# Kernel optimization log

Measured on AMD Instinct MI355X. Metric: run time of the kernel, lower is better.

## Reference

```python
import jax, jax.numpy as jnp
import numpy as np

L, D, H, DR, KF = 2, 256, 8, 64, 4   # n_layer, d_model, n_head, d_rpe, k_feedforward
B, S, T = 2, 256, 256
LN_EPS = 1e-5


def _ln(x, g, b):
    m = jnp.mean(x, -1, keepdims=True)
    v = jnp.mean((x - m) ** 2, -1, keepdims=True)
    return (x - m) * jax.lax.rsqrt(v + LN_EPS) * g + b


def _attn_rpe(q_in, kv_in, rpe, tgt_mask, wq, bq, wk, bk, wv, bv, wo, bo, wr, br):
    # RPE-biased multi-head cross attention: rpe -> (rpe_k, rpe_v) added per (src,tgt) pair.
    Bq, Sq, _ = q_in.shape
    Tk = kv_in.shape[1]
    Dh = D // H
    q = (q_in @ wq + bq).reshape(Bq, Sq, H, Dh)
    k = (kv_in @ wk + bk).reshape(Bq, Tk, H, Dh)
    v = (kv_in @ wv + bv).reshape(Bq, Tk, H, Dh)
    r = rpe @ wr + br                                   # [B,S,T,2D]
    rk, rv = jnp.split(r, 2, axis=-1)
    rk = rk.reshape(Bq, Sq, Tk, H, Dh)
    rv = rv.reshape(Bq, Sq, Tk, H, Dh)
    scale = 1.0 / np.sqrt(Dh).astype(np.float32)
    scores = (jnp.einsum('bshd,bthd->bhst', q, k)
              + jnp.einsum('bshd,bsthd->bhst', q, rk)) * scale
    scores = jnp.where(tgt_mask[:, None, None, :], -jnp.inf, scores)
    w = jax.nn.softmax(scores, axis=-1)                 # [B,H,S,T]
    out = (jnp.einsum('bhst,bthd->bshd', w, v)
           + jnp.einsum('bhst,bsthd->bshd', w, rv))
    return out.reshape(Bq, Sq, D) @ wo + bo


def _forward(src, tgt, rpe, src_padding_mask, tgt_padding_mask, p):
    for i in range(L):  # loop over n_layer (structurally distinct params)
        s2 = _ln(src, p['ln1_g'][i], p['ln1_b'][i])
        tn = _ln(tgt, p['lnt_g'][i], p['lnt_b'][i])
        a = _attn_rpe(s2, tn, rpe, tgt_padding_mask,
                      p['wq'][i], p['bq'][i], p['wk'][i], p['bk'][i],
                      p['wv'][i], p['bv'][i], p['wo'][i], p['bo'][i],
                      p['wr'][i], p['br'][i])
        src = src + a
        s2 = _ln(src, p['ln2_g'][i], p['ln2_b'][i])
        s2 = jax.nn.relu(s2 @ p['w1'][i] + p['b1'][i]) @ p['w2'][i] + p['b2'][i]
        src = src + s2
        src = jnp.where(src_padding_mask[:, :, None], 0.0, src)
    return src


def setup_inputs() -> dict:
    key = jax.random.key(0)
    ks = jax.random.split(key, 16)
    f = lambda k, shp: (0.02 * jax.random.normal(k, shp)).astype(jnp.float32)
    return {
        'src': jax.random.normal(ks[0], (B, S, D), jnp.float32),
        'tgt': jax.random.normal(ks[1], (B, T, D), jnp.float32),
        'rpe': jax.random.normal(ks[2], (B, S, T, DR), jnp.float32),
        'src_padding_mask': jax.random.bernoulli(ks[3], 0.05, (B, S)),
        'tgt_padding_mask': jax.random.bernoulli(ks[4], 0.1, (B, T)),
        'ln1_g': jnp.ones((L, D), jnp.float32), 'ln1_b': jnp.zeros((L, D), jnp.float32),
        'lnt_g': jnp.ones((L, D), jnp.float32), 'lnt_b': jnp.zeros((L, D), jnp.float32),
        'ln2_g': jnp.ones((L, D), jnp.float32), 'ln2_b': jnp.zeros((L, D), jnp.float32),
        'wq': f(ks[5], (L, D, D)), 'bq': jnp.zeros((L, D), jnp.float32),
        'wk': f(ks[6], (L, D, D)), 'bk': jnp.zeros((L, D), jnp.float32),
        'wv': f(ks[7], (L, D, D)), 'bv': jnp.zeros((L, D), jnp.float32),
        'wo': f(ks[8], (L, D, D)), 'bo': jnp.zeros((L, D), jnp.float32),
        'wr': f(ks[9], (L, DR, 2 * D)), 'br': jnp.zeros((L, 2 * D), jnp.float32),
        'w1': f(ks[10], (L, D, KF * D)), 'b1': jnp.zeros((L, KF * D), jnp.float32),
        'w2': f(ks[11], (L, KF * D, D)), 'b2': jnp.zeros((L, D), jnp.float32),
    }


def reference(src, tgt, rpe, src_padding_mask, tgt_padding_mask,
              ln1_g, ln1_b, lnt_g, lnt_b, ln2_g, ln2_b,
              wq, bq, wk, bk, wv, bv, wo, bo, wr, br, w1, b1, w2, b2):
    p = dict(ln1_g=ln1_g, ln1_b=ln1_b, lnt_g=lnt_g, lnt_b=lnt_b,
             ln2_g=ln2_g, ln2_b=ln2_b, wq=wq, bq=bq, wk=wk, bk=bk,
             wv=wv, bv=bv, wo=wo, bo=bo, wr=wr, br=br,
             w1=w1, b1=b1, w2=w2, b2=b2)
    return _forward(src, tgt, rpe, src_padding_mask, tgt_padding_mask, p)
```

## Files before the change

### kernel.cpp

```cpp
#include <hip/hip_runtime.h>
#include <math.h>

#define DMODEL 256
#define NH 8
#define DH 32
#define NEG_INF -1e30f


__device__ __forceinline__ void stage_B64(const float* __restrict__ Bw, int ldb, int n0,
                                          float (*__restrict__ Bs)[64])
{
  int tid = threadIdx.x;
#pragma unroll
  for (int i = 0; i < 32; ++i) {
    int idx = tid + 128 * i;
    int k = idx >> 4, c = (idx & 15) << 2;
    *(float4*)&Bs[k][c] = *(const float4*)(Bw + (size_t)k * ldb + n0 + c);
  }
}

__device__ __forceinline__ void stage_A_copy(const float* __restrict__ A, int lda,
                                             int m0, int kbeg,
                                             float (*__restrict__ As)[36])
{
  int tid = threadIdx.x;
  int r = tid >> 2, p = tid & 3;
  const float* row = A + (size_t)(m0 + r) * lda + kbeg + p * 64;
#pragma unroll
  for (int j = 0; j < 16; ++j) {
    float4 v = *(const float4*)(row + j * 4);
    int k = p * 64 + j * 4;
    As[k + 0][r] = v.x; As[k + 1][r] = v.y; As[k + 2][r] = v.z; As[k + 3][r] = v.w;
  }
}

__device__ __forceinline__ void stage_A_ln(const float* __restrict__ Xsrc, int m0,
                                           const float* __restrict__ g,
                                           const float* __restrict__ b,
                                           float (*__restrict__ As)[36])
{
  int tid = threadIdx.x;
  int r = tid >> 2, p = tid & 3;
  const float* row = Xsrc + (size_t)(m0 + r) * DMODEL + p * 64;
  float4 v[16];
  float s = 0.f, ss = 0.f;
#pragma unroll
  for (int j = 0; j < 16; ++j) {
    v[j] = *(const float4*)(row + j * 4);
    s  += v[j].x + v[j].y + v[j].z + v[j].w;
    ss += v[j].x * v[j].x + v[j].y * v[j].y + v[j].z * v[j].z + v[j].w * v[j].w;
  }
  s  += __shfl_xor(s, 1);  s  += __shfl_xor(s, 2);
  ss += __shfl_xor(ss, 1); ss += __shfl_xor(ss, 2);
  float mean = s * (1.0f / 256.0f);
  float var  = ss * (1.0f / 256.0f) - mean * mean;
  float rstd = rsqrtf(var + 1e-5f);
#pragma unroll
  for (int j = 0; j < 16; ++j) {
    float4 gg = *(const float4*)(g + p * 64 + j * 4);
    float4 bb = *(const float4*)(b + p * 64 + j * 4);
    int k = p * 64 + j * 4;
    As[k + 0][r] = (v[j].x - mean) * rstd * gg.x + bb.x;
    As[k + 1][r] = (v[j].y - mean) * rstd * gg.y + bb.y;
    As[k + 2][r] = (v[j].z - mean) * rstd * gg.z + bb.z;
    As[k + 3][r] = (v[j].w - mean) * rstd * gg.w + bb.w;
  }
}

__device__ __forceinline__ void gemm_compute(const float (*__restrict__ As)[36],
                                             const float (*__restrict__ Bs)[64],
                                             float acc[4][4])
{
  int tid = threadIdx.x;
  int tx = tid & 15, ty = tid >> 4;
#pragma unroll 8
  for (int k = 0; k < 256; ++k) {
    float4 a  = *(const float4*)&As[k][ty * 4];
    float4 bv = *(const float4*)&Bs[k][tx * 4];
    acc[0][0] = fmaf(a.x, bv.x, acc[0][0]); acc[0][1] = fmaf(a.x, bv.y, acc[0][1]);
    acc[0][2] = fmaf(a.x, bv.z, acc[0][2]); acc[0][3] = fmaf(a.x, bv.w, acc[0][3]);
    acc[1][0] = fmaf(a.y, bv.x, acc[1][0]); acc[1][1] = fmaf(a.y, bv.y, acc[1][1]);
    acc[1][2] = fmaf(a.y, bv.z, acc[1][2]); acc[1][3] = fmaf(a.y, bv.w, acc[1][3]);
    acc[2][0] = fmaf(a.z, bv.x, acc[2][0]); acc[2][1] = fmaf(a.z, bv.y, acc[2][1]);
    acc[2][2] = fmaf(a.z, bv.z, acc[2][2]); acc[2][3] = fmaf(a.z, bv.w, acc[2][3]);
    acc[3][0] = fmaf(a.w, bv.x, acc[3][0]); acc[3][1] = fmaf(a.w, bv.y, acc[3][1]);
    acc[3][2] = fmaf(a.w, bv.z, acc[3][2]); acc[3][3] = fmaf(a.w, bv.w, acc[3][3]);
  }
}

__global__ __launch_bounds__(128) void qkv_kernel(
    const float* __restrict__ srcin, const float* __restrict__ tgt,
    const float* __restrict__ ln1g, const float* __restrict__ ln1b,
    const float* __restrict__ lntg, const float* __restrict__ lntb,
    const float* __restrict__ wq, const float* __restrict__ wk, const float* __restrict__ wv,
    const float* __restrict__ bq, const float* __restrict__ bk, const float* __restrict__ bv,
    float* __restrict__ Qb, float* __restrict__ Kb, float* __restrict__ Vb)
{
  __shared__ __align__(16) float As[256][36];
  __shared__ __align__(16) float Bs[256][64];
  int z = blockIdx.z;
  int m0 = blockIdx.y * 32, n0 = blockIdx.x * 64;
  const float* Bw = (z == 0) ? wq : (z == 1) ? wk : wv;
  stage_B64(Bw, DMODEL, n0, Bs);
  if (z == 0) stage_A_ln(srcin, m0, ln1g, ln1b, As);
  else        stage_A_ln(tgt,   m0, lntg, lntb, As);
  __syncthreads();
  float acc[4][4] = {};
  gemm_compute(As, Bs, acc);
  const float* bias = (z == 0) ? bq : (z == 1) ? bk : bv;
  int tid = threadIdx.x, tx = tid & 15, ty = tid >> 4;
  int c0 = n0 + tx * 4;
  float4 bias4 = *(const float4*)(bias + c0);
  const float scale = 0.1767766952966369f;
#pragma unroll
  for (int i = 0; i < 4; ++i) {
    int m = m0 + ty * 4 + i;
    float4 r;
    r.x = acc[i][0] + bias4.x;
    r.y = acc[i][1] + bias4.y;
    r.z = acc[i][2] + bias4.z;
    r.w = acc[i][3] + bias4.w;
    if (z == 0) {
      r.x *= scale; r.y *= scale; r.z *= scale; r.w *= scale;
      *(float4*)&Qb[m * DMODEL + c0] = r;
    } else {
      int b = m >> 8, t = m & 255, h = c0 >> 5, d0 = c0 & 31;
      float* dst = ((z == 1) ? Kb : Vb) + (size_t)(b * NH + h) * 8192 + t * DH + d0;
      *(float4*)dst = r;
    }
  }
}

__global__ __launch_bounds__(128) void wo_kernel(
    const float* __restrict__ AO, const float* __restrict__ wo,
    const float* __restrict__ srcin, const float* __restrict__ bo,
    float* __restrict__ X)
{
  __shared__ __align__(16) float As[256][36];
  __shared__ __align__(16) float Bs[256][64];
  int m0 = blockIdx.y * 32, n0 = blockIdx.x * 64;
  stage_B64(wo, DMODEL, n0, Bs);
  stage_A_copy(AO, DMODEL, m0, 0, As);
  __syncthreads();
  float acc[4][4] = {};
  gemm_compute(As, Bs, acc);
  int tid = threadIdx.x, tx = tid & 15, ty = tid >> 4;
  int c0 = n0 + tx * 4;
  float4 bov = *(const float4*)(bo + c0);
#pragma unroll
  for (int i = 0; i < 4; ++i) {
    int m = m0 + ty * 4 + i;
    float4 sv = *(const float4*)(srcin + (size_t)m * DMODEL + c0);
    float4 r;
    r.x = sv.x + bov.x + acc[i][0];
    r.y = sv.y + bov.y + acc[i][1];
    r.z = sv.z + bov.z + acc[i][2];
    r.w = sv.w + bov.w + acc[i][3];
    *(float4*)&X[(size_t)m * DMODEL + c0] = r;
  }
}

__global__ __launch_bounds__(128) void ff1_kernel(
    const float* __restrict__ X, const float* __restrict__ ln2g, const float* __restrict__ ln2b,
    const float* __restrict__ w1, const float* __restrict__ b1,
    const float* __restrict__ b2, const int* __restrict__ smask,
    float* __restrict__ H1, float* __restrict__ outb)
{
  __shared__ __align__(16) float As[256][36];
  __shared__ __align__(16) float Bs[256][64];
  int m0 = blockIdx.y * 32, n0 = blockIdx.x * 64;
  stage_B64(w1, 1024, n0, Bs);
  stage_A_ln(X, m0, ln2g, ln2b, As);
  if (blockIdx.x == 0) {
    int tid = threadIdx.x;
    int r = tid >> 2, p = tid & 3;
    int m = m0 + r;
    float mm = (smask[m] != 0) ? 0.0f : 1.0f;
#pragma unroll
    for (int j = 0; j < 16; ++j) {
      float4 xv  = *(const float4*)(X  + (size_t)m * DMODEL + p * 64 + j * 4);
      float4 b2v = *(const float4*)(b2 + p * 64 + j * 4);
      float4 o;
      o.x = mm * (xv.x + b2v.x); o.y = mm * (xv.y + b2v.y);
      o.z = mm * (xv.z + b2v.z); o.w = mm * (xv.w + b2v.w);
      *(float4*)(outb + (size_t)m * DMODEL + p * 64 + j * 4) = o;
    }
  }
  __syncthreads();
  float acc[4][4] = {};
  gemm_compute(As, Bs, acc);
  int tid = threadIdx.x, tx = tid & 15, ty = tid >> 4;
  int c0 = n0 + tx * 4;
  float4 b1v = *(const float4*)(b1 + c0);
#pragma unroll
  for (int i = 0; i < 4; ++i) {
    int m = m0 + ty * 4 + i;
    float4 r;
    r.x = fmaxf(acc[i][0] + b1v.x, 0.0f);
    r.y = fmaxf(acc[i][1] + b1v.y, 0.0f);
    r.z = fmaxf(acc[i][2] + b1v.z, 0.0f);
    r.w = fmaxf(acc[i][3] + b1v.w, 0.0f);
    *(float4*)&H1[(size_t)m * 1024 + c0] = r;
  }
}

__global__ __launch_bounds__(128) void ff2_kernel(
    const float* __restrict__ H1, const float* __restrict__ w2,
    const int* __restrict__ smask, float* __restrict__ outb)
{
  __shared__ __align__(16) float As[256][36];
  __shared__ __align__(16) float Bs[256][64];
  int m0 = blockIdx.y * 32, n0 = blockIdx.x * 64;
  int kbeg = blockIdx.z * 256;
  stage_B64(w2 + (size_t)kbeg * DMODEL, DMODEL, n0, Bs);
  stage_A_copy(H1, 1024, m0, kbeg, As);
  __syncthreads();
  float acc[4][4] = {};
  gemm_compute(As, Bs, acc);
  int tid = threadIdx.x, tx = tid & 15, ty = tid >> 4;
  int c0 = n0 + tx * 4;
#pragma unroll
  for (int i = 0; i < 4; ++i) {
    int m = m0 + ty * 4 + i;
    if (smask[m] == 0) {
      atomicAdd(&outb[(size_t)m * DMODEL + c0 + 0], acc[i][0]);
      atomicAdd(&outb[(size_t)m * DMODEL + c0 + 1], acc[i][1]);
      atomicAdd(&outb[(size_t)m * DMODEL + c0 + 2], acc[i][2]);
      atomicAdd(&outb[(size_t)m * DMODEL + c0 + 3], acc[i][3]);
    }
  }
}

__global__ __launch_bounds__(256) void attn_kernel(
    const float* __restrict__ Qb, const float* __restrict__ Kb, const float* __restrict__ Vb,
    const float* __restrict__ rpe, const int* __restrict__ tmask,
    const float* __restrict__ wrl, const float* __restrict__ brl,
    float* __restrict__ AO)
{
  __shared__ float Ks[256][32];
  __shared__ float Vt[32][260];
  __shared__ float ps[4][256];
  __shared__ float qs[16][32];
  __shared__ float wks[5][32];
  __shared__ float wvs[5][32];
  int bid = blockIdx.x;
  int b = bid >> 7, h = (bid >> 4) & 7, s0 = (bid & 15) << 4;
  int tid = threadIdx.x;
  const float* Kp = Kb + (size_t)(b * NH + h) * 8192;
  const float* Vp = Vb + (size_t)(b * NH + h) * 8192;
  {
    int t = tid;
    const float4* kr = (const float4*)(Kp + t * DH);
    const float4* vr = (const float4*)(Vp + t * DH);
    int sw = t & 7;
#pragma unroll
    for (int c = 0; c < 8; ++c) {
      float4 k4 = kr[c];
      *(float4*)&Ks[t][(c ^ sw) * 4] = k4;
    }
#pragma unroll
    for (int c = 0; c < 8; ++c) {
      float4 v4 = vr[c];
      Vt[c*4+0][t] = v4.x; Vt[c*4+1][t] = v4.y; Vt[c*4+2][t] = v4.z; Vt[c*4+3][t] = v4.w;
    }
  }
  if (tid < 160) {
    int j = tid >> 5, d = tid & 31;
    wks[j][d] = (j < 4) ? wrl[j * 512 + h * DH + d]       : brl[h * DH + d];
    wvs[j][d] = (j < 4) ? wrl[j * 512 + 256 + h * DH + d] : brl[256 + h * DH + d];
  }
  if (tid >= 128) {
    int u = tid - 128;
    int rr = u >> 3, cc = u & 7;
    *(float4*)&qs[rr][cc*4] =
        *(const float4*)&Qb[(b * 256 + s0 + rr) * DMODEL + h * DH + cc * 4];
  }
  __syncthreads();

  int w = tid >> 6, lane = tid & 63;
  int msk[4];
#pragma unroll
  for (int it = 0; it < 4; ++it) msk[it] = tmask[b * 256 + it * 64 + lane];

  for (int i = 0; i < 4; ++i) {
    int sl = w * 4 + i;
    int s = s0 + sl;
    float4 q4[8];
#pragma unroll
    for (int c = 0; c < 8; ++c) q4[c] = *(const float4*)&qs[sl][c * 4];
    float qw[4]; float qbr = 0.0f;
#pragma unroll
    for (int j = 0; j < 4; ++j) {
      float t0 = 0;
#pragma unroll
      for (int c = 0; c < 8; ++c) {
        float4 wv4 = *(const float4*)&wks[j][c * 4];
        t0 += q4[c].x*wv4.x + q4[c].y*wv4.y + q4[c].z*wv4.z + q4[c].w*wv4.w;
      }
      qw[j] = t0;
    }
#pragma unroll
    for (int c = 0; c < 8; ++c) {
      float4 wv4 = *(const float4*)&wks[4][c * 4];
      qbr += q4[c].x*wv4.x + q4[c].y*wv4.y + q4[c].z*wv4.z + q4[c].w*wv4.w;
    }
    const float4* rp4 = (const float4*)(rpe + (size_t)(b * 256 + s) * 1024);
    float sc[4]; float4 rr[4];
#pragma unroll
    for (int it = 0; it < 4; ++it) {
      int t = it * 64 + lane;
      int sw = t & 7;
      float sv = 0;
#pragma unroll
      for (int c = 0; c < 8; ++c) {
        float4 k4 = *(const float4*)&Ks[t][(c ^ sw) * 4];
        sv = fmaf(q4[c].x, k4.x, sv); sv = fmaf(q4[c].y, k4.y, sv);
        sv = fmaf(q4[c].z, k4.z, sv); sv = fmaf(q4[c].w, k4.w, sv);
      }
      float4 rv = rp4[t];
      rr[it] = rv;
      sv += rv.x*qw[0] + rv.y*qw[1] + rv.z*qw[2] + rv.w*qw[3] + qbr;
      if (msk[it] != 0) sv = NEG_INF;
      sc[it] = sv;
    }
    float mval = fmaxf(fmaxf(sc[0], sc[1]), fmaxf(sc[2], sc[3]));
#pragma unroll
    for (int off = 32; off >= 1; off >>= 1) mval = fmaxf(mval, __shfl_xor(mval, off));
    float p[4], lsum = 0;
#pragma unroll
    for (int it = 0; it < 4; ++it) { p[it] = __expf(sc[it] - mval); lsum += p[it]; }
    float wj0 = 0, wj1 = 0, wj2 = 0, wj3 = 0;
#pragma unroll
    for (int it = 0; it < 4; ++it) {
      wj0 = fmaf(p[it], rr[it].x, wj0);
      wj1 = fmaf(p[it], rr[it].y, wj1);
      wj2 = fmaf(p[it], rr[it].z, wj2);
      wj3 = fmaf(p[it], rr[it].w, wj3);
    }
#pragma unroll
    for (int off = 32; off >= 1; off >>= 1) {
      lsum += __shfl_xor(lsum, off);
      wj0 += __shfl_xor(wj0, off);
      wj1 += __shfl_xor(wj1, off);
      wj2 += __shfl_xor(wj2, off);
      wj3 += __shfl_xor(wj3, off);
    }
#pragma unroll
    for (int it = 0; it < 4; ++it) ps[w][it * 64 + lane] = p[it];
    int g = lane >> 5, d = lane & 31;
    float o = 0;
#pragma unroll
    for (int n = 0; n < 32; ++n) {
      int t = g * 128 + n * 4;
      float4 p4 = *(const float4*)&ps[w][t];
      float4 v4 = *(const float4*)&Vt[d][t];
      o += p4.x*v4.x + p4.y*v4.y + p4.z*v4.z + p4.w*v4.w;
    }
    o += __shfl_xor(o, 32);
    float corr = wj0 * wvs[0][d] + wj1 * wvs[1][d] + wj2 * wvs[2][d] + wj3 * wvs[3][d];
    float oval = (o + corr) / lsum + wvs[4][d];
    if (lane < 32) AO[(b * 256 + s) * DMODEL + h * DH + d] = oval;
  }
}

extern "C" void kernel_launch(void* const* d_in, const int* in_sizes, int n_in,
                              void* d_out, int out_size, void* d_ws, size_t ws_size,
                              hipStream_t stream)
{
  const float* src  = (const float*)d_in[0];
  const float* tgt  = (const float*)d_in[1];
  const float* rpe  = (const float*)d_in[2];
  const int*   smask = (const int*)d_in[3];
  const int*   tmask = (const int*)d_in[4];
  const float* ln1g = (const float*)d_in[5];
  const float* ln1b = (const float*)d_in[6];
  const float* lntg = (const float*)d_in[7];
  const float* lntb = (const float*)d_in[8];
  const float* ln2g = (const float*)d_in[9];
  const float* ln2b = (const float*)d_in[10];
  const float* wq = (const float*)d_in[11];
  const float* bq = (const float*)d_in[12];
  const float* wk = (const float*)d_in[13];
  const float* bk = (const float*)d_in[14];
  const float* wv = (const float*)d_in[15];
  const float* bv = (const float*)d_in[16];
  const float* wo = (const float*)d_in[17];
  const float* bo = (const float*)d_in[18];
  const float* wr = (const float*)d_in[19];
  const float* br = (const float*)d_in[20];
  const float* w1 = (const float*)d_in[21];
  const float* b1 = (const float*)d_in[22];
  const float* w2 = (const float*)d_in[23];
  const float* b2 = (const float*)d_in[24];

  float* w    = (float*)d_ws;
  float* Qb   = w;
  float* Kb   = w + 131072;
  float* Vb   = w + 262144;
  float* AO   = w + 393216;
  float* X    = w + 524288;
  float* SRC1 = w + 655360;
  float* H1   = w + 786432;

  for (int l = 0; l < 2; ++l) {
    const float* srcin = l ? SRC1 : src;
    float* outb = l ? (float*)d_out : SRC1;
    qkv_kernel<<<dim3(4, 16, 3), 128, 0, stream>>>(
        srcin, tgt, ln1g + l*256, ln1b + l*256, lntg + l*256, lntb + l*256,
        wq + l*65536, wk + l*65536, wv + l*65536,
        bq + l*256, bk + l*256, bv + l*256, Qb, Kb, Vb);
    attn_kernel<<<256, 256, 0, stream>>>(Qb, Kb, Vb, rpe, tmask,
                                         wr + l*2048, br + l*512, AO);
    wo_kernel<<<dim3(4, 16), 128, 0, stream>>>(AO, wo + l*65536, srcin, bo + l*256, X);
    ff1_kernel<<<dim3(16, 16), 128, 0, stream>>>(X, ln2g + l*256, ln2b + l*256,
                                                 w1 + l*262144, b1 + l*1024,
                                                 b2 + l*256, smask, H1, outb);
    ff2_kernel<<<dim3(4, 16, 4), 128, 0, stream>>>(H1, w2 + l*262144, smask, outb);
  }
}
```

Baseline: 273.8 us.

## Fuse all per-layer kernels into one cooperative persistent megakernel with grid syncs

Replaces the ten separate launches (five kernels per layer across two layers) with a single cooperative kernel of 256 blocks. Each stage (QKV projection, attention, output projection, FF1, FF2) runs as a phase, and grid.sync() separates the phases. The aim is to remove per-launch overhead and the idle gaps between dependent kernels. In exchange, blocks sit idle in the smaller phases, the GEMM phases use only 128 of 256 threads for compute, and the multi-kernel path is kept as a fallback if the cooperative launch fails.

```diff
diff --git a/kernel.cpp b/kernel.cpp
--- a/kernel.cpp
+++ b/kernel.cpp
@@ -1,71 +1,13 @@
 #include <hip/hip_runtime.h>
+#include <hip/hip_cooperative_groups.h>
 #include <math.h>
+
+namespace cg = cooperative_groups;
 
 #define DMODEL 256
 #define NH 8
 #define DH 32
 #define NEG_INF -1e30f
-
-
-__device__ __forceinline__ void stage_B64(const float* __restrict__ Bw, int ldb, int n0,
-                                          float (*__restrict__ Bs)[64])
-{
-  int tid = threadIdx.x;
-#pragma unroll
-  for (int i = 0; i < 32; ++i) {
-    int idx = tid + 128 * i;
-    int k = idx >> 4, c = (idx & 15) << 2;
-    *(float4*)&Bs[k][c] = *(const float4*)(Bw + (size_t)k * ldb + n0 + c);
-  }
-}
-
-__device__ __forceinline__ void stage_A_copy(const float* __restrict__ A, int lda,
-                                             int m0, int kbeg,
-                                             float (*__restrict__ As)[36])
-{
-  int tid = threadIdx.x;
-  int r = tid >> 2, p = tid & 3;
-  const float* row = A + (size_t)(m0 + r) * lda + kbeg + p * 64;
-#pragma unroll
-  for (int j = 0; j < 16; ++j) {
-    float4 v = *(const float4*)(row + j * 4);
-    int k = p * 64 + j * 4;
-    As[k + 0][r] = v.x; As[k + 1][r] = v.y; As[k + 2][r] = v.z; As[k + 3][r] = v.w;
-  }
-}
-
-__device__ __forceinline__ void stage_A_ln(const float* __restrict__ Xsrc, int m0,
-                                           const float* __restrict__ g,
-                                           const float* __restrict__ b,
-                                           float (*__restrict__ As)[36])
-{
-  int tid = threadIdx.x;
-  int r = tid >> 2, p = tid & 3;
-  const float* row = Xsrc + (size_t)(m0 + r) * DMODEL + p * 64;
-  float4 v[16];
-  float s = 0.f, ss = 0.f;
-#pragma unroll
-  for (int j = 0; j < 16; ++j) {
-    v[j] = *(const float4*)(row + j * 4);
-    s  += v[j].x + v[j].y + v[j].z + v[j].w;
-    ss += v[j].x * v[j].x + v[j].y * v[j].y + v[j].z * v[j].z + v[j].w * v[j].w;
-  }
-  s  += __shfl_xor(s, 1);  s  += __shfl_xor(s, 2);
-  ss += __shfl_xor(ss, 1); ss += __shfl_xor(ss, 2);
-  float mean = s * (1.0f / 256.0f);
-  float var  = ss * (1.0f / 256.0f) - mean * mean;
-  float rstd = rsqrtf(var + 1e-5f);
-#pragma unroll
-  for (int j = 0; j < 16; ++j) {
-    float4 gg = *(const float4*)(g + p * 64 + j * 4);
-    float4 bb = *(const float4*)(b + p * 64 + j * 4);
-    int k = p * 64 + j * 4;
-    As[k + 0][r] = (v[j].x - mean) * rstd * gg.x + bb.x;
-    As[k + 1][r] = (v[j].y - mean) * rstd * gg.y + bb.y;
-    As[k + 2][r] = (v[j].z - mean) * rstd * gg.z + bb.z;
-    As[k + 3][r] = (v[j].w - mean) * rstd * gg.w + bb.w;
-  }
-}
 
 __device__ __forceinline__ void gemm_compute(const float (*__restrict__ As)[36],
                                              const float (*__restrict__ Bs)[64],
@@ -85,6 +27,418 @@
     acc[2][2] = fmaf(a.z, bv.z, acc[2][2]); acc[2][3] = fmaf(a.z, bv.w, acc[2][3]);
     acc[3][0] = fmaf(a.w, bv.x, acc[3][0]); acc[3][1] = fmaf(a.w, bv.y, acc[3][1]);
     acc[3][2] = fmaf(a.w, bv.z, acc[3][2]); acc[3][3] = fmaf(a.w, bv.w, acc[3][3]);
+  }
+}
+
+__device__ __forceinline__ void stageB_256(const float* __restrict__ Bw, int ldb, int n0,
+                                           float (*__restrict__ Bs)[64])
+{
+  int tid = threadIdx.x;
+#pragma unroll
+  for (int i = 0; i < 16; ++i) {
+    int idx = tid + 256 * i;
+    int k = idx >> 4, c = (idx & 15) << 2;
+    *(float4*)&Bs[k][c] = *(const float4*)(Bw + (size_t)k * ldb + n0 + c);
+  }
+}
+
+__device__ __forceinline__ void stageA_copy_256(const float* __restrict__ A, int lda,
+                                                int m0, int kbeg,
+                                                float (*__restrict__ As)[36])
+{
+  int tid = threadIdx.x;
+  int r = tid >> 3, p = tid & 7;
+  const float* row = A + (size_t)(m0 + r) * lda + kbeg + p * 32;
+#pragma unroll
+  for (int j = 0; j < 8; ++j) {
+    float4 v = *(const float4*)(row + j * 4);
+    int k = p * 32 + j * 4;
+    As[k + 0][r] = v.x; As[k + 1][r] = v.y; As[k + 2][r] = v.z; As[k + 3][r] = v.w;
+  }
+}
+
+__device__ __forceinline__ void stageA_ln_256(const float* __restrict__ Xsrc, int m0,
+                                              const float* __restrict__ g,
+                                              const float* __restrict__ b,
+                                              float (*__restrict__ As)[36])
+{
+  int tid = threadIdx.x;
+  int r = tid >> 3, p = tid & 7;
+  const float* row = Xsrc + (size_t)(m0 + r) * DMODEL + p * 32;
+  float4 v[8];
+  float s = 0.f, ss = 0.f;
+#pragma unroll
+  for (int j = 0; j < 8; ++j) {
+    v[j] = *(const float4*)(row + j * 4);
+    s  += v[j].x + v[j].y + v[j].z + v[j].w;
+    ss += v[j].x * v[j].x + v[j].y * v[j].y + v[j].z * v[j].z + v[j].w * v[j].w;
+  }
+  s  += __shfl_xor(s, 1);  s  += __shfl_xor(s, 2);  s  += __shfl_xor(s, 4);
+  ss += __shfl_xor(ss, 1); ss += __shfl_xor(ss, 2); ss += __shfl_xor(ss, 4);
+  float mean = s * (1.0f / 256.0f);
+  float var  = ss * (1.0f / 256.0f) - mean * mean;
+  float rstd = rsqrtf(var + 1e-5f);
+#pragma unroll
+  for (int j = 0; j < 8; ++j) {
+    float4 gg = *(const float4*)(g + p * 32 + j * 4);
+    float4 bb = *(const float4*)(b + p * 32 + j * 4);
+    int k = p * 32 + j * 4;
+    As[k + 0][r] = (v[j].x - mean) * rstd * gg.x + bb.x;
+    As[k + 1][r] = (v[j].y - mean) * rstd * gg.y + bb.y;
+    As[k + 2][r] = (v[j].z - mean) * rstd * gg.z + bb.z;
+    As[k + 3][r] = (v[j].w - mean) * rstd * gg.w + bb.w;
+  }
+}
+
+struct MegaParams {
+  const float* src; const float* tgt; const float* rpe;
+  const int* smask; const int* tmask;
+  const float* ln1g; const float* ln1b; const float* lntg; const float* lntb;
+  const float* ln2g; const float* ln2b;
+  const float* wq; const float* bq; const float* wk; const float* bk;
+  const float* wv; const float* bv; const float* wo; const float* bo;
+  const float* wr; const float* br; const float* w1; const float* b1;
+  const float* w2; const float* b2;
+  float* out; float* Qb; float* Kb; float* Vb; float* AO; float* X; float* SRC1; float* H1;
+};
+
+__global__ __launch_bounds__(256) void mega_kernel(MegaParams p)
+{
+  cg::grid_group grid = cg::this_grid();
+  __shared__ __align__(16) float smem[25600];
+  float (*As)[36]  = reinterpret_cast<float (*)[36]>(smem);
+  float (*Bs)[64]  = reinterpret_cast<float (*)[64]>(smem + 9216);
+  float (*Ks)[32]  = reinterpret_cast<float (*)[32]>(smem);
+  float (*Vt)[260] = reinterpret_cast<float (*)[260]>(smem + 8192);
+  float (*ps)[256] = reinterpret_cast<float (*)[256]>(smem + 16512);
+  float (*qs)[32]  = reinterpret_cast<float (*)[32]>(smem + 17536);
+  float (*wks)[32] = reinterpret_cast<float (*)[32]>(smem + 18048);
+  float (*wvs)[32] = reinterpret_cast<float (*)[32]>(smem + 18208);
+  int bid = blockIdx.x, tid = threadIdx.x;
+
+  for (int l = 0; l < 2; ++l) {
+    const float* srcin = l ? p.SRC1 : p.src;
+    float* outb = l ? p.out : p.SRC1;
+    const float* wq = p.wq + l * 65536;  const float* bq = p.bq + l * 256;
+    const float* wk = p.wk + l * 65536;  const float* bk = p.bk + l * 256;
+    const float* wv = p.wv + l * 65536;  const float* bv = p.bv + l * 256;
+    const float* wo = p.wo + l * 65536;  const float* bo = p.bo + l * 256;
+    const float* wr = p.wr + l * 2048;   const float* br = p.br + l * 512;
+    const float* w1 = p.w1 + l * 262144; const float* b1 = p.b1 + l * 1024;
+    const float* w2 = p.w2 + l * 262144; const float* b2 = p.b2 + l * 256;
+    const float* ln1g = p.ln1g + l * 256; const float* ln1b = p.ln1b + l * 256;
+    const float* lntg = p.lntg + l * 256; const float* lntb = p.lntb + l * 256;
+    const float* ln2g = p.ln2g + l * 256; const float* ln2b = p.ln2b + l * 256;
+
+    if (bid < 192) {
+      int x = bid & 3, y = (bid >> 2) & 15, z = bid >> 6;
+      int m0 = y * 32, n0 = x * 64;
+      const float* Bw = (z == 0) ? wq : (z == 1) ? wk : wv;
+      stageB_256(Bw, DMODEL, n0, Bs);
+      if (z == 0) stageA_ln_256(srcin, m0, ln1g, ln1b, As);
+      else        stageA_ln_256(p.tgt, m0, lntg, lntb, As);
+      __syncthreads();
+      if (tid < 128) {
+        float acc[4][4] = {};
+        gemm_compute(As, Bs, acc);
+        const float* bias = (z == 0) ? bq : (z == 1) ? bk : bv;
+        int tx = tid & 15, ty = tid >> 4;
+        int c0 = n0 + tx * 4;
+        float4 bias4 = *(const float4*)(bias + c0);
+        const float scale = 0.1767766952966369f;
+#pragma unroll
+        for (int i = 0; i < 4; ++i) {
+          int m = m0 + ty * 4 + i;
+          float4 r;
+          r.x = acc[i][0] + bias4.x;
+          r.y = acc[i][1] + bias4.y;
+          r.z = acc[i][2] + bias4.z;
+          r.w = acc[i][3] + bias4.w;
+          if (z == 0) {
+            r.x *= scale; r.y *= scale; r.z *= scale; r.w *= scale;
+            *(float4*)&p.Qb[m * DMODEL + c0] = r;
+          } else {
+            int b_ = m >> 8, t = m & 255, h = c0 >> 5, d0 = c0 & 31;
+            float* dst = ((z == 1) ? p.Kb : p.Vb) + (size_t)(b_ * NH + h) * 8192 + t * DH + d0;
+            *(float4*)dst = r;
+          }
+        }
+      }
+    }
+    grid.sync();
+
+    {
+      int ab = bid >> 7, h = (bid >> 4) & 7, s0 = (bid & 15) << 4;
+      const float* Kp = p.Kb + (size_t)(ab * NH + h) * 8192;
+      const float* Vp = p.Vb + (size_t)(ab * NH + h) * 8192;
+      {
+        int t = tid;
+        const float4* kr = (const float4*)(Kp + t * DH);
+        const float4* vr = (const float4*)(Vp + t * DH);
+        int sw = t & 7;
+#pragma unroll
+        for (int c = 0; c < 8; ++c) {
+          float4 k4 = kr[c];
+          *(float4*)&Ks[t][(c ^ sw) * 4] = k4;
+        }
+#pragma unroll
+        for (int c = 0; c < 8; ++c) {
+          float4 v4 = vr[c];
+          Vt[c*4+0][t] = v4.x; Vt[c*4+1][t] = v4.y; Vt[c*4+2][t] = v4.z; Vt[c*4+3][t] = v4.w;
+        }
+      }
+      if (tid < 160) {
+        int j = tid >> 5, d = tid & 31;
+        wks[j][d] = (j < 4) ? wr[j * 512 + h * DH + d]       : br[h * DH + d];
+        wvs[j][d] = (j < 4) ? wr[j * 512 + 256 + h * DH + d] : br[256 + h * DH + d];
+      }
+      if (tid >= 128) {
+        int u = tid - 128;
+        int rr_ = u >> 3, cc = u & 7;
+        *(float4*)&qs[rr_][cc*4] =
+            *(const float4*)&p.Qb[(ab * 256 + s0 + rr_) * DMODEL + h * DH + cc * 4];
+      }
+      __syncthreads();
+
+      int w = tid >> 6, lane = tid & 63;
+      int msk[4];
+#pragma unroll
+      for (int it = 0; it < 4; ++it) msk[it] = p.tmask[ab * 256 + it * 64 + lane];
+
+      for (int i = 0; i < 4; ++i) {
+        int sl = w * 4 + i;
+        int s = s0 + sl;
+        float4 q4[8];
+#pragma unroll
+        for (int c = 0; c < 8; ++c) q4[c] = *(const float4*)&qs[sl][c * 4];
+        float qw[4]; float qbr = 0.0f;
+#pragma unroll
+        for (int j = 0; j < 4; ++j) {
+          float t0 = 0;
+#pragma unroll
+          for (int c = 0; c < 8; ++c) {
+            float4 wv4 = *(const float4*)&wks[j][c * 4];
+            t0 += q4[c].x*wv4.x + q4[c].y*wv4.y + q4[c].z*wv4.z + q4[c].w*wv4.w;
+          }
+          qw[j] = t0;
+        }
+#pragma unroll
+        for (int c = 0; c < 8; ++c) {
+          float4 wv4 = *(const float4*)&wks[4][c * 4];
+          qbr += q4[c].x*wv4.x + q4[c].y*wv4.y + q4[c].z*wv4.z + q4[c].w*wv4.w;
+        }
+        const float4* rp4 = (const float4*)(p.rpe + (size_t)(ab * 256 + s) * 1024);
+        float sc[4]; float4 rr[4];
+#pragma unroll
+        for (int it = 0; it < 4; ++it) {
+          int t = it * 64 + lane;
+          int sw = t & 7;
+          float sv = 0;
+#pragma unroll
+          for (int c = 0; c < 8; ++c) {
+            float4 k4 = *(const float4*)&Ks[t][(c ^ sw) * 4];
+            sv = fmaf(q4[c].x, k4.x, sv); sv = fmaf(q4[c].y, k4.y, sv);
+            sv = fmaf(q4[c].z, k4.z, sv); sv = fmaf(q4[c].w, k4.w, sv);
+          }
+          float4 rv = rp4[t];
+          rr[it] = rv;
+          sv += rv.x*qw[0] + rv.y*qw[1] + rv.z*qw[2] + rv.w*qw[3] + qbr;
+          if (msk[it] != 0) sv = NEG_INF;
+          sc[it] = sv;
+        }
+        float mval = fmaxf(fmaxf(sc[0], sc[1]), fmaxf(sc[2], sc[3]));
+#pragma unroll
+        for (int off = 32; off >= 1; off >>= 1) mval = fmaxf(mval, __shfl_xor(mval, off));
+        float pr[4], lsum = 0;
+#pragma unroll
+        for (int it = 0; it < 4; ++it) { pr[it] = __expf(sc[it] - mval); lsum += pr[it]; }
+        float wj0 = 0, wj1 = 0, wj2 = 0, wj3 = 0;
+#pragma unroll
+        for (int it = 0; it < 4; ++it) {
+          wj0 = fmaf(pr[it], rr[it].x, wj0);
+          wj1 = fmaf(pr[it], rr[it].y, wj1);
+          wj2 = fmaf(pr[it], rr[it].z, wj2);
+          wj3 = fmaf(pr[it], rr[it].w, wj3);
+        }
+#pragma unroll
+        for (int off = 32; off >= 1; off >>= 1) {
+          lsum += __shfl_xor(lsum, off);
+          wj0 += __shfl_xor(wj0, off);
+          wj1 += __shfl_xor(wj1, off);
+          wj2 += __shfl_xor(wj2, off);
+          wj3 += __shfl_xor(wj3, off);
+        }
+#pragma unroll
+        for (int it = 0; it < 4; ++it) ps[w][it * 64 + lane] = pr[it];
+        int g = lane >> 5, d = lane & 31;
+        float o = 0;
+#pragma unroll
+        for (int n = 0; n < 32; ++n) {
+          int t = g * 128 + n * 4;
+          float4 p4 = *(const float4*)&ps[w][t];
+          float4 v4 = *(const float4*)&Vt[d][t];
+          o += p4.x*v4.x + p4.y*v4.y + p4.z*v4.z + p4.w*v4.w;
+        }
+        o += __shfl_xor(o, 32);
+        float corr = wj0 * wvs[0][d] + wj1 * wvs[1][d] + wj2 * wvs[2][d] + wj3 * wvs[3][d];
+        float oval = (o + corr) / lsum + wvs[4][d];
+        if (lane < 32) p.AO[(ab * 256 + s) * DMODEL + h * DH + d] = oval;
+      }
+    }
+    grid.sync();
+
+    if (bid < 64) {
+      int x = bid & 3, y = bid >> 2;
+      int m0 = y * 32, n0 = x * 64;
+      stageB_256(wo, DMODEL, n0, Bs);
+      stageA_copy_256(p.AO, DMODEL, m0, 0, As);
+      __syncthreads();
+      if (tid < 128) {
+        float acc[4][4] = {};
+        gemm_compute(As, Bs, acc);
+        int tx = tid & 15, ty = tid >> 4;
+        int c0 = n0 + tx * 4;
+        float4 bov = *(const float4*)(bo + c0);
+#pragma unroll
+        for (int i = 0; i < 4; ++i) {
+          int m = m0 + ty * 4 + i;
+          float4 sv = *(const float4*)(srcin + (size_t)m * DMODEL + c0);
+          float4 r;
+          r.x = sv.x + bov.x + acc[i][0];
+          r.y = sv.y + bov.y + acc[i][1];
+          r.z = sv.z + bov.z + acc[i][2];
+          r.w = sv.w + bov.w + acc[i][3];
+          *(float4*)&p.X[(size_t)m * DMODEL + c0] = r;
+        }
+      }
+    }
+    grid.sync();
+
+    {
+      int x = bid & 15, y = bid >> 4;
+      int m0 = y * 32, n0 = x * 64;
+      stageB_256(w1, 1024, n0, Bs);
+      stageA_ln_256(p.X, m0, ln2g, ln2b, As);
+      if (x == 0 && tid < 128) {
+        int r = tid >> 2, pq = tid & 3;
+        int m = m0 + r;
+        float mm = (p.smask[m] != 0) ? 0.0f : 1.0f;
+#pragma unroll
+        for (int j = 0; j < 16; ++j) {
+          float4 xv  = *(const float4*)(p.X + (size_t)m * DMODEL + pq * 64 + j * 4);
+          float4 b2v = *(const float4*)(b2 + pq * 64 + j * 4);
+          float4 o;
+          o.x = mm * (xv.x + b2v.x); o.y = mm * (xv.y + b2v.y);
+          o.z = mm * (xv.z + b2v.z); o.w = mm * (xv.w + b2v.w);
+          *(float4*)(outb + (size_t)m * DMODEL + pq * 64 + j * 4) = o;
+        }
+      }
+      __syncthreads();
+      if (tid < 128) {
+        float acc[4][4] = {};
+        gemm_compute(As, Bs, acc);
+        int tx = tid & 15, ty = tid >> 4;
+        int c0 = n0 + tx * 4;
+        float4 b1v = *(const float4*)(b1 + c0);
+#pragma unroll
+        for (int i = 0; i < 4; ++i) {
+          int m = m0 + ty * 4 + i;
+          float4 r;
+          r.x = fmaxf(acc[i][0] + b1v.x, 0.0f);
+          r.y = fmaxf(acc[i][1] + b1v.y, 0.0f);
+          r.z = fmaxf(acc[i][2] + b1v.z, 0.0f);
+          r.w = fmaxf(acc[i][3] + b1v.w, 0.0f);
+          *(float4*)&p.H1[(size_t)m * 1024 + c0] = r;
+        }
+      }
+    }
+    grid.sync();
+
+    {
+      int x = bid & 3, y = (bid >> 2) & 15, z = bid >> 6;
+      int m0 = y * 32, n0 = x * 64;
+      int kbeg = z * 256;
+      stageB_256(w2 + (size_t)kbeg * DMODEL, DMODEL, n0, Bs);
+      stageA_copy_256(p.H1, 1024, m0, kbeg, As);
+      __syncthreads();
+      if (tid < 128) {
+        float acc[4][4] = {};
+        gemm_compute(As, Bs, acc);
+        int tx = tid & 15, ty = tid >> 4;
+        int c0 = n0 + tx * 4;
+#pragma unroll
+        for (int i = 0; i < 4; ++i) {
+          int m = m0 + ty * 4 + i;
+          if (p.smask[m] == 0) {
+            atomicAdd(&outb[(size_t)m * DMODEL + c0 + 0], acc[i][0]);
+            atomicAdd(&outb[(size_t)m * DMODEL + c0 + 1], acc[i][1]);
+            atomicAdd(&outb[(size_t)m * DMODEL + c0 + 2], acc[i][2]);
+            atomicAdd(&outb[(size_t)m * DMODEL + c0 + 3], acc[i][3]);
+          }
+        }
+      }
+    }
+    if (l == 0) grid.sync();
+  }
+}
+
+__device__ __forceinline__ void stage_B64(const float* __restrict__ Bw, int ldb, int n0,
+                                          float (*__restrict__ Bs)[64])
+{
+  int tid = threadIdx.x;
+#pragma unroll
+  for (int i = 0; i < 32; ++i) {
+    int idx = tid + 128 * i;
+    int k = idx >> 4, c = (idx & 15) << 2;
+    *(float4*)&Bs[k][c] = *(const float4*)(Bw + (size_t)k * ldb + n0 + c);
+  }
+}
+
+__device__ __forceinline__ void stage_A_copy(const float* __restrict__ A, int lda,
+                                             int m0, int kbeg,
+                                             float (*__restrict__ As)[36])
+{
+  int tid = threadIdx.x;
+  int r = tid >> 2, p = tid & 3;
+  const float* row = A + (size_t)(m0 + r) * lda + kbeg + p * 64;
+#pragma unroll
+  for (int j = 0; j < 16; ++j) {
+    float4 v = *(const float4*)(row + j * 4);
+    int k = p * 64 + j * 4;
+    As[k + 0][r] = v.x; As[k + 1][r] = v.y; As[k + 2][r] = v.z; As[k + 3][r] = v.w;
+  }
+}
+
+__device__ __forceinline__ void stage_A_ln(const float* __restrict__ Xsrc, int m0,
+                                           const float* __restrict__ g,
+                                           const float* __restrict__ b,
+                                           float (*__restrict__ As)[36])
+{
+  int tid = threadIdx.x;
+  int r = tid >> 2, p = tid & 3;
+  const float* row = Xsrc + (size_t)(m0 + r) * DMODEL + p * 64;
+  float4 v[16];
+  float s = 0.f, ss = 0.f;
+#pragma unroll
+  for (int j = 0; j < 16; ++j) {
+    v[j] = *(const float4*)(row + j * 4);
+    s  += v[j].x + v[j].y + v[j].z + v[j].w;
+    ss += v[j].x * v[j].x + v[j].y * v[j].y + v[j].z * v[j].z + v[j].w * v[j].w;
+  }
+  s  += __shfl_xor(s, 1);  s  += __shfl_xor(s, 2);
+  ss += __shfl_xor(ss, 1); ss += __shfl_xor(ss, 2);
+  float mean = s * (1.0f / 256.0f);
+  float var  = ss * (1.0f / 256.0f) - mean * mean;
+  float rstd = rsqrtf(var + 1e-5f);
+#pragma unroll
+  for (int j = 0; j < 16; ++j) {
+    float4 gg = *(const float4*)(g + p * 64 + j * 4);
+    float4 bb = *(const float4*)(b + p * 64 + j * 4);
+    int k = p * 64 + j * 4;
+    As[k + 0][r] = (v[j].x - mean) * rstd * gg.x + bb.x;
+    As[k + 1][r] = (v[j].y - mean) * rstd * gg.y + bb.y;
+    As[k + 2][r] = (v[j].z - mean) * rstd * gg.z + bb.z;
+    As[k + 3][r] = (v[j].w - mean) * rstd * gg.w + bb.w;
   }
 }
 
@@ -402,19 +756,35 @@
   float* SRC1 = w + 655360;
   float* H1   = w + 786432;
 
-  for (int l = 0; l < 2; ++l) {
-    const float* srcin = l ? SRC1 : src;
-    float* outb = l ? (float*)d_out : SRC1;
-    qkv_kernel<<<dim3(4, 16, 3), 128, 0, stream>>>(
-        srcin, tgt, ln1g + l*256, ln1b + l*256, lntg + l*256, lntb + l*256,
-        wq + l*65536, wk + l*65536, wv + l*65536,
-        bq + l*256, bk + l*256, bv + l*256, Qb, Kb, Vb);
-    attn_kernel<<<256, 256, 0, stream>>>(Qb, Kb, Vb, rpe, tmask,
-                                         wr + l*2048, br + l*512, AO);
-    wo_kernel<<<dim3(4, 16), 128, 0, stream>>>(AO, wo + l*65536, srcin, bo + l*256, X);
-    ff1_kernel<<<dim3(16, 16), 128, 0, stream>>>(X, ln2g + l*256, ln2b + l*256,
-                                                 w1 + l*262144, b1 + l*1024,
-                                                 b2 + l*256, smask, H1, outb);
-    ff2_kernel<<<dim3(4, 16, 4), 128, 0, stream>>>(H1, w2 + l*262144, smask, outb);
-  }
-}
+  MegaParams mp;
+  mp.src = src; mp.tgt = tgt; mp.rpe = rpe; mp.smask = smask; mp.tmask = tmask;
+  mp.ln1g = ln1g; mp.ln1b = ln1b; mp.lntg = lntg; mp.lntb = lntb;
+  mp.ln2g = ln2g; mp.ln2b = ln2b;
+  mp.wq = wq; mp.bq = bq; mp.wk = wk; mp.bk = bk; mp.wv = wv; mp.bv = bv;
+  mp.wo = wo; mp.bo = bo; mp.wr = wr; mp.br = br;
+  mp.w1 = w1; mp.b1 = b1; mp.w2 = w2; mp.b2 = b2;
+  mp.out = (float*)d_out;
+  mp.Qb = Qb; mp.Kb = Kb; mp.Vb = Vb; mp.AO = AO; mp.X = X; mp.SRC1 = SRC1; mp.H1 = H1;
+
+  void* args[] = { &mp };
+  hipError_t err = hipLaunchCooperativeKernel((const void*)mega_kernel,
+                                              dim3(256), dim3(256), args, 0, stream);
+  if (err != hipSuccess) {
+    (void)hipGetLastError();
+    for (int l = 0; l < 2; ++l) {
+      const float* srcin = l ? SRC1 : src;
+      float* outb = l ? (float*)d_out : SRC1;
+      qkv_kernel<<<dim3(4, 16, 3), 128, 0, stream>>>(
+          srcin, tgt, ln1g + l*256, ln1b + l*256, lntg + l*256, lntb + l*256,
+          wq + l*65536, wk + l*65536, wv + l*65536,
+          bq + l*256, bk + l*256, bv + l*256, Qb, Kb, Vb);
+      attn_kernel<<<256, 256, 0, stream>>>(Qb, Kb, Vb, rpe, tmask,
+                                           wr + l*2048, br + l*512, AO);
+      wo_kernel<<<dim3(4, 16), 128, 0, stream>>>(AO, wo + l*65536, srcin, bo + l*256, X);
+      ff1_kernel<<<dim3(16, 16), 128, 0, stream>>>(X, ln2g + l*256, ln2b + l*256,
+                                                   w1 + l*262144, b1 + l*1024,
+                                                   b2 + l*256, smask, H1, outb);
+      ff2_kernel<<<dim3(4, 16, 4), 128, 0, stream>>>(H1, w2 + l*262144, smask, outb);
+    }
+  }
+}
```

New measurement: 612.4 us. 2.24x slower.

## Double-buffer GEMM K-loop in 64-wide chunks with register prefetch

Applied to the files above, without the earlier changes.

Replaces the single full-K shared-memory staging in the qkv, wo, ff1 and ff2 GEMM kernels with a two-stage double-buffered pipeline over four 64-wide K chunks. The next chunk's weights and activations are prefetched into registers while the current chunk is computed. This cuts shared memory per block from about 100KB to about 51KB, which should allow more blocks per CU and hide global load latency. The cost is extra barriers and register pressure from the prefetch buffers.

```diff
diff --git a/kernel.cpp b/kernel.cpp
--- a/kernel.cpp
+++ b/kernel.cpp
@@ -6,75 +6,14 @@
 #define DH 32
 #define NEG_INF -1e30f
 
-
-__device__ __forceinline__ void stage_B64(const float* __restrict__ Bw, int ldb, int n0,
-                                          float (*__restrict__ Bs)[64])
-{
-  int tid = threadIdx.x;
-#pragma unroll
-  for (int i = 0; i < 32; ++i) {
-    int idx = tid + 128 * i;
-    int k = idx >> 4, c = (idx & 15) << 2;
-    *(float4*)&Bs[k][c] = *(const float4*)(Bw + (size_t)k * ldb + n0 + c);
-  }
-}
-
-__device__ __forceinline__ void stage_A_copy(const float* __restrict__ A, int lda,
-                                             int m0, int kbeg,
-                                             float (*__restrict__ As)[36])
-{
-  int tid = threadIdx.x;
-  int r = tid >> 2, p = tid & 3;
-  const float* row = A + (size_t)(m0 + r) * lda + kbeg + p * 64;
-#pragma unroll
-  for (int j = 0; j < 16; ++j) {
-    float4 v = *(const float4*)(row + j * 4);
-    int k = p * 64 + j * 4;
-    As[k + 0][r] = v.x; As[k + 1][r] = v.y; As[k + 2][r] = v.z; As[k + 3][r] = v.w;
-  }
-}
-
-__device__ __forceinline__ void stage_A_ln(const float* __restrict__ Xsrc, int m0,
-                                           const float* __restrict__ g,
-                                           const float* __restrict__ b,
-                                           float (*__restrict__ As)[36])
-{
-  int tid = threadIdx.x;
-  int r = tid >> 2, p = tid & 3;
-  const float* row = Xsrc + (size_t)(m0 + r) * DMODEL + p * 64;
-  float4 v[16];
-  float s = 0.f, ss = 0.f;
-#pragma unroll
-  for (int j = 0; j < 16; ++j) {
-    v[j] = *(const float4*)(row + j * 4);
-    s  += v[j].x + v[j].y + v[j].z + v[j].w;
-    ss += v[j].x * v[j].x + v[j].y * v[j].y + v[j].z * v[j].z + v[j].w * v[j].w;
-  }
-  s  += __shfl_xor(s, 1);  s  += __shfl_xor(s, 2);
-  ss += __shfl_xor(ss, 1); ss += __shfl_xor(ss, 2);
-  float mean = s * (1.0f / 256.0f);
-  float var  = ss * (1.0f / 256.0f) - mean * mean;
-  float rstd = rsqrtf(var + 1e-5f);
-#pragma unroll
-  for (int j = 0; j < 16; ++j) {
-    float4 gg = *(const float4*)(g + p * 64 + j * 4);
-    float4 bb = *(const float4*)(b + p * 64 + j * 4);
-    int k = p * 64 + j * 4;
-    As[k + 0][r] = (v[j].x - mean) * rstd * gg.x + bb.x;
-    As[k + 1][r] = (v[j].y - mean) * rstd * gg.y + bb.y;
-    As[k + 2][r] = (v[j].z - mean) * rstd * gg.z + bb.z;
-    As[k + 3][r] = (v[j].w - mean) * rstd * gg.w + bb.w;
-  }
-}
-
-__device__ __forceinline__ void gemm_compute(const float (*__restrict__ As)[36],
-                                             const float (*__restrict__ Bs)[64],
-                                             float acc[4][4])
+__device__ __forceinline__ void gemm_chunk(const float (*__restrict__ As)[36],
+                                           const float (*__restrict__ Bs)[64],
+                                           float acc[4][4])
 {
   int tid = threadIdx.x;
   int tx = tid & 15, ty = tid >> 4;
 #pragma unroll 8
-  for (int k = 0; k < 256; ++k) {
+  for (int k = 0; k < 64; ++k) {
     float4 a  = *(const float4*)&As[k][ty * 4];
     float4 bv = *(const float4*)&Bs[k][tx * 4];
     acc[0][0] = fmaf(a.x, bv.x, acc[0][0]); acc[0][1] = fmaf(a.x, bv.y, acc[0][1]);
@@ -88,6 +27,149 @@
   }
 }
 
+__device__ __forceinline__ void gemm_ln(
+    const float* __restrict__ Xsrc,
+    const float* __restrict__ g, const float* __restrict__ b,
+    const float* __restrict__ Bw, int ldb, int m0, int n0,
+    float (*__restrict__ As)[64][36], float (*__restrict__ Bs)[64][64],
+    float acc[4][4])
+{
+  int tid = threadIdx.x;
+  int r = tid >> 2, p = tid & 3;
+  const float* row = Xsrc + (size_t)(m0 + r) * DMODEL;
+  float4 v[16];
+  float s = 0.f, ss = 0.f;
+#pragma unroll
+  for (int j = 0; j < 16; ++j) {
+    int kg = (j >> 2) * 64 + p * 16 + (j & 3) * 4;
+    v[j] = *(const float4*)(row + kg);
+    s  += v[j].x + v[j].y + v[j].z + v[j].w;
+    ss += v[j].x * v[j].x + v[j].y * v[j].y + v[j].z * v[j].z + v[j].w * v[j].w;
+  }
+  s  += __shfl_xor(s, 1);  s  += __shfl_xor(s, 2);
+  ss += __shfl_xor(ss, 1); ss += __shfl_xor(ss, 2);
+  float mean = s * (1.0f / 256.0f);
+  float var  = ss * (1.0f / 256.0f) - mean * mean;
+  float rstd = rsqrtf(var + 1e-5f);
+#pragma unroll
+  for (int j = 0; j < 16; ++j) {
+    v[j].x = (v[j].x - mean) * rstd;
+    v[j].y = (v[j].y - mean) * rstd;
+    v[j].z = (v[j].z - mean) * rstd;
+    v[j].w = (v[j].w - mean) * rstd;
+  }
+#pragma unroll
+  for (int i = 0; i < 8; ++i) {
+    int idx = tid + 128 * i;
+    int k = idx >> 4, c = (idx & 15) << 2;
+    *(float4*)&Bs[0][k][c] = *(const float4*)(Bw + (size_t)k * ldb + n0 + c);
+  }
+#pragma unroll
+  for (int j = 0; j < 4; ++j) {
+    int kl = p * 16 + j * 4;
+    float4 gg = *(const float4*)(g + kl);
+    float4 bb = *(const float4*)(b + kl);
+    As[0][kl + 0][r] = v[j].x * gg.x + bb.x;
+    As[0][kl + 1][r] = v[j].y * gg.y + bb.y;
+    As[0][kl + 2][r] = v[j].z * gg.z + bb.z;
+    As[0][kl + 3][r] = v[j].w * gg.w + bb.w;
+  }
+  __syncthreads();
+  for (int c = 0; c < 4; ++c) {
+    int cur = c & 1;
+    float4 breg[8];
+    if (c < 3) {
+      int kb = (c + 1) * 64;
+#pragma unroll
+      for (int i = 0; i < 8; ++i) {
+        int idx = tid + 128 * i;
+        int k = idx >> 4, cc = (idx & 15) << 2;
+        breg[i] = *(const float4*)(Bw + (size_t)(kb + k) * ldb + n0 + cc);
+      }
+    }
+    gemm_chunk(As[cur], Bs[cur], acc);
+    if (c < 3) {
+      int nxt = cur ^ 1;
+      int kb = (c + 1) * 64;
+#pragma unroll
+      for (int i = 0; i < 8; ++i) {
+        int idx = tid + 128 * i;
+        int k = idx >> 4, cc = (idx & 15) << 2;
+        *(float4*)&Bs[nxt][k][cc] = breg[i];
+      }
+#pragma unroll
+      for (int j = 0; j < 4; ++j) {
+        int kl = p * 16 + j * 4;
+        float4 gg = *(const float4*)(g + kb + kl);
+        float4 bb = *(const float4*)(b + kb + kl);
+        float4 vv = v[(c + 1) * 4 + j];
+        As[nxt][kl + 0][r] = vv.x * gg.x + bb.x;
+        As[nxt][kl + 1][r] = vv.y * gg.y + bb.y;
+        As[nxt][kl + 2][r] = vv.z * gg.z + bb.z;
+        As[nxt][kl + 3][r] = vv.w * gg.w + bb.w;
+      }
+      __syncthreads();
+    }
+  }
+}
+
+__device__ __forceinline__ void gemm_copy(
+    const float* __restrict__ A, int lda, int kbeg,
+    const float* __restrict__ Bw, int ldb, int m0, int n0,
+    float (*__restrict__ As)[64][36], float (*__restrict__ Bs)[64][64],
+    float acc[4][4])
+{
+  int tid = threadIdx.x;
+  int r = tid >> 2, p = tid & 3;
+  const float* arow = A + (size_t)(m0 + r) * lda + kbeg;
+#pragma unroll
+  for (int i = 0; i < 8; ++i) {
+    int idx = tid + 128 * i;
+    int k = idx >> 4, c = (idx & 15) << 2;
+    *(float4*)&Bs[0][k][c] = *(const float4*)(Bw + (size_t)k * ldb + n0 + c);
+  }
+#pragma unroll
+  for (int j = 0; j < 4; ++j) {
+    int kl = p * 16 + j * 4;
+    float4 vv = *(const float4*)(arow + kl);
+    As[0][kl + 0][r] = vv.x; As[0][kl + 1][r] = vv.y;
+    As[0][kl + 2][r] = vv.z; As[0][kl + 3][r] = vv.w;
+  }
+  __syncthreads();
+  for (int c = 0; c < 4; ++c) {
+    int cur = c & 1;
+    float4 breg[8]; float4 areg[4];
+    if (c < 3) {
+      int kb = (c + 1) * 64;
+#pragma unroll
+      for (int i = 0; i < 8; ++i) {
+        int idx = tid + 128 * i;
+        int k = idx >> 4, cc = (idx & 15) << 2;
+        breg[i] = *(const float4*)(Bw + (size_t)(kb + k) * ldb + n0 + cc);
+      }
+#pragma unroll
+      for (int j = 0; j < 4; ++j) areg[j] = *(const float4*)(arow + kb + p * 16 + j * 4);
+    }
+    gemm_chunk(As[cur], Bs[cur], acc);
+    if (c < 3) {
+      int nxt = cur ^ 1;
+#pragma unroll
+      for (int i = 0; i < 8; ++i) {
+        int idx = tid + 128 * i;
+        int k = idx >> 4, cc = (idx & 15) << 2;
+        *(float4*)&Bs[nxt][k][cc] = breg[i];
+      }
+#pragma unroll
+      for (int j = 0; j < 4; ++j) {
+        int kl = p * 16 + j * 4;
+        As[nxt][kl + 0][r] = areg[j].x; As[nxt][kl + 1][r] = areg[j].y;
+        As[nxt][kl + 2][r] = areg[j].z; As[nxt][kl + 3][r] = areg[j].w;
+      }
+      __syncthreads();
+    }
+  }
+}
+
 __global__ __launch_bounds__(128) void qkv_kernel(
     const float* __restrict__ srcin, const float* __restrict__ tgt,
     const float* __restrict__ ln1g, const float* __restrict__ ln1b,
@@ -96,17 +178,14 @@
     const float* __restrict__ bq, const float* __restrict__ bk, const float* __restrict__ bv,
     float* __restrict__ Qb, float* __restrict__ Kb, float* __restrict__ Vb)
 {
-  __shared__ __align__(16) float As[256][36];
-  __shared__ __align__(16) float Bs[256][64];
+  __shared__ __align__(16) float As[2][64][36];
+  __shared__ __align__(16) float Bs[2][64][64];
   int z = blockIdx.z;
   int m0 = blockIdx.y * 32, n0 = blockIdx.x * 64;
   const float* Bw = (z == 0) ? wq : (z == 1) ? wk : wv;
-  stage_B64(Bw, DMODEL, n0, Bs);
-  if (z == 0) stage_A_ln(srcin, m0, ln1g, ln1b, As);
-  else        stage_A_ln(tgt,   m0, lntg, lntb, As);
-  __syncthreads();
   float acc[4][4] = {};
-  gemm_compute(As, Bs, acc);
+  if (z == 0) gemm_ln(srcin, ln1g, ln1b, Bw, DMODEL, m0, n0, As, Bs, acc);
+  else        gemm_ln(tgt, lntg, lntb, Bw, DMODEL, m0, n0, As, Bs, acc);
   const float* bias = (z == 0) ? bq : (z == 1) ? bk : bv;
   int tid = threadIdx.x, tx = tid & 15, ty = tid >> 4;
   int c0 = n0 + tx * 4;
@@ -136,14 +215,11 @@
     const float* __restrict__ srcin, const float* __restrict__ bo,
     float* __restrict__ X)
 {
-  __shared__ __align__(16) float As[256][36];
-  __shared__ __align__(16) float Bs[256][64];
+  __shared__ __align__(16) float As[2][64][36];
+  __shared__ __align__(16) float Bs[2][64][64];
   int m0 = blockIdx.y * 32, n0 = blockIdx.x * 64;
-  stage_B64(wo, DMODEL, n0, Bs);
-  stage_A_copy(AO, DMODEL, m0, 0, As);
-  __syncthreads();
   float acc[4][4] = {};
-  gemm_compute(As, Bs, acc);
+  gemm_copy(AO, DMODEL, 0, wo, DMODEL, m0, n0, As, Bs, acc);
   int tid = threadIdx.x, tx = tid & 15, ty = tid >> 4;
   int c0 = n0 + tx * 4;
   float4 bov = *(const float4*)(bo + c0);
@@ -166,29 +242,44 @@
     const float* __restrict__ b2, const int* __restrict__ smask,
     float* __restrict__ H1, float* __restrict__ outb)
 {
-  __shared__ __align__(16) float As[256][36];
-  __shared__ __align__(16) float Bs[256][64];
+  __shared__ __align__(16) float As[2][64][36];
+  __shared__ __align__(16) float Bs[2][64][64];
   int m0 = blockIdx.y * 32, n0 = blockIdx.x * 64;
-  stage_B64(w1, 1024, n0, Bs);
-  stage_A_ln(X, m0, ln2g, ln2b, As);
   if (blockIdx.x == 0) {
     int tid = threadIdx.x;
-    int r = tid >> 2, p = tid & 3;
+    int r = tid >> 2, pq = tid & 3;
     int m = m0 + r;
     float mm = (smask[m] != 0) ? 0.0f : 1.0f;
 #pragma unroll
-    for (int j = 0; j < 16; ++j) {
-      float4 xv  = *(const float4*)(X  + (size_t)m * DMODEL + p * 64 + j * 4);
-      float4 b2v = *(const float4*)(b2 + p * 64 + j * 4);
+    for (int j = 0; j < 4; ++j) {
+      float4 xv  = *(const float4*)(X  + (size_t)m * DMODEL + pq * 64 + j * 16);
+      float4 b2v = *(const float4*)(b2 + pq * 64 + j * 16);
       float4 o;
       o.x = mm * (xv.x + b2v.x); o.y = mm * (xv.y + b2v.y);
       o.z = mm * (xv.z + b2v.z); o.w = mm * (xv.w + b2v.w);
-      *(float4*)(outb + (size_t)m * DMODEL + p * 64 + j * 4) = o;
-    }
-  }
-  __syncthreads();
+      *(float4*)(outb + (size_t)m * DMODEL + pq * 64 + j * 16) = o;
+      float4 xv2  = *(const float4*)(X  + (size_t)m * DMODEL + pq * 64 + j * 16 + 4);
+      float4 b2v2 = *(const float4*)(b2 + pq * 64 + j * 16 + 4);
+      float4 o2;
+      o2.x = mm * (xv2.x + b2v2.x); o2.y = mm * (xv2.y + b2v2.y);
+      o2.z = mm * (xv2.z + b2v2.z); o2.w = mm * (xv2.w + b2v2.w);
+      *(float4*)(outb + (size_t)m * DMODEL + pq * 64 + j * 16 + 4) = o2;
+      float4 xv3  = *(const float4*)(X  + (size_t)m * DMODEL + pq * 64 + j * 16 + 8);
+      float4 b2v3 = *(const float4*)(b2 + pq * 64 + j * 16 + 8);
+      float4 o3;
+      o3.x = mm * (xv3.x + b2v3.x); o3.y = mm * (xv3.y + b2v3.y);
+      o3.z = mm * (xv3.z + b2v3.z); o3.w = mm * (xv3.w + b2v3.w);
+      *(float4*)(outb + (size_t)m * DMODEL + pq * 64 + j * 16 + 8) = o3;
+      float4 xv4  = *(const float4*)(X  + (size_t)m * DMODEL + pq * 64 + j * 16 + 12);
+      float4 b2v4 = *(const float4*)(b2 + pq * 64 + j * 16 + 12);
+      float4 o4;
+      o4.x = mm * (xv4.x + b2v4.x); o4.y = mm * (xv4.y + b2v4.y);
+      o4.z = mm * (xv4.z + b2v4.z); o4.w = mm * (xv4.w + b2v4.w);
+      *(float4*)(outb + (size_t)m * DMODEL + pq * 64 + j * 16 + 12) = o4;
+    }
+  }
   float acc[4][4] = {};
-  gemm_compute(As, Bs, acc);
+  gemm_ln(X, ln2g, ln2b, w1, 1024, m0, n0, As, Bs, acc);
   int tid = threadIdx.x, tx = tid & 15, ty = tid >> 4;
   int c0 = n0 + tx * 4;
   float4 b1v = *(const float4*)(b1 + c0);
@@ -208,15 +299,12 @@
     const float* __restrict__ H1, const float* __restrict__ w2,
     const int* __restrict__ smask, float* __restrict__ outb)
 {
-  __shared__ __align__(16) float As[256][36];
-  __shared__ __align__(16) float Bs[256][64];
+  __shared__ __align__(16) float As[2][64][36];
+  __shared__ __align__(16) float Bs[2][64][64];
   int m0 = blockIdx.y * 32, n0 = blockIdx.x * 64;
   int kbeg = blockIdx.z * 256;
-  stage_B64(w2 + (size_t)kbeg * DMODEL, DMODEL, n0, Bs);
-  stage_A_copy(H1, 1024, m0, kbeg, As);
-  __syncthreads();
   float acc[4][4] = {};
-  gemm_compute(As, Bs, acc);
+  gemm_copy(H1, 1024, kbeg, w2 + (size_t)kbeg * DMODEL, DMODEL, m0, n0, As, Bs, acc);
   int tid = threadIdx.x, tx = tid & 15, ty = tid >> 4;
   int c0 = n0 + tx * 4;
 #pragma unroll
```

Result: no change. 271.9 us (-0.7%).
